# Kernel tuning notes

Measured on AMD Instinct MI355X. Metric: run time of the kernel, lower is better.

## Reference

```python
import jax, jax.numpy as jnp
import numpy as np

B, S, D, L = 32, 4096, 1024, 1

def setup_inputs() -> dict:
    key = jax.random.key(0)
    ks = jax.random.split(key, 9)
    sc = 1.0 / np.sqrt(D)
    return {
        "encoder_outputs": jax.random.normal(ks[0], (B, S, D), jnp.float32),
        "decoder_hidden_state": jax.random.normal(ks[1], (L, B, D), jnp.float32),
        "attn_mask": jax.random.randint(ks[2], (B, S), 0, 2) > 0,
        "Wa_w": jax.random.normal(ks[3], (D, D), jnp.float32) * sc,
        "Wa_b": jax.random.normal(ks[4], (D,), jnp.float32) * sc,
        "Ua_w": jax.random.normal(ks[5], (D, D), jnp.float32) * sc,
        "Ua_b": jax.random.normal(ks[6], (D,), jnp.float32) * sc,
        "Va_w": jax.random.normal(ks[7], (1, D), jnp.float32) * sc,
        "Va_b": jax.random.normal(ks[8], (1,), jnp.float32) * sc,
    }

def reference(encoder_outputs, decoder_hidden_state, attn_mask,
              Wa_w, Wa_b, Ua_w, Ua_b, Va_w, Va_b):
    # Ua(decoder_hidden_state): [L,B,D] -> transpose(0,1) -> [B,L,D] -> keep layer 0 -> [B,1,D]
    dec = jnp.einsum('lbd,ed->lbe', decoder_hidden_state, Ua_w) + Ua_b
    dec = jnp.transpose(dec, (1, 0, 2))[:, 0:1, :]            # [B,1,D]
    # Wa(encoder_outputs): [B,S,D]
    enc = jnp.einsum('bsd,ed->bse', encoder_outputs, Wa_w) + Wa_b
    # scores = Va(tanh(enc + dec)) -> [B,S,1] -> [B,1,S]
    scores = jnp.einsum('bsd,od->bso', jnp.tanh(enc + dec), Va_w) + Va_b
    scores = scores[:, :, 0][:, None, :]                      # [B,1,S]
    scores = jnp.where(attn_mask[:, None, :], scores, -jnp.inf)
    weights = jax.nn.softmax(scores, axis=-1)
    return weights
```

## Files before the change

### kernel.cpp

```cpp
#include <hip/hip_runtime.h>
#include <math.h>

#define D_DIM 1024
#define S_DIM 4096
#define B_DIM 32
#define M_TOTAL (B_DIM * S_DIM)

#define KQ   128
#define NPH  8

using short8 = __attribute__((ext_vector_type(8))) short;
using f32x4  = __attribute__((ext_vector_type(4))) float;

static __device__ __forceinline__ unsigned short f2bf(float x) {
    unsigned int u = __float_as_uint(x);
    u += 0x7fffu + ((u >> 16) & 1u);
    return (unsigned short)(u >> 16);
}

static __device__ __forceinline__ float fast_tanh(float x) {
    float e2 = __expf(2.0f * x);
    return 1.0f - 2.0f * __builtin_amdgcn_rcpf(e2 + 1.0f);
}

__global__ __launch_bounds__(256) void mask_detect_kernel(
        const unsigned int* __restrict__ m, int* __restrict__ flag) {
    __shared__ unsigned int red[4];
    int t = threadIdx.x;
    unsigned int acc = 0;
    for (int i = t; i < 32768; i += 256) acc |= (m[i] & 0xFFFFFF00u);
    #pragma unroll
    for (int k = 1; k <= 32; k <<= 1) acc |= __shfl_xor(acc, k, 64);
    if ((t & 63) == 0) red[t >> 6] = acc;
    __syncthreads();
    if (t == 0) flag[0] = ((red[0] | red[1] | red[2] | red[3]) != 0) ? 1 : 0;
}

__global__ __launch_bounds__(256) void wconv_kernel(
        const float* __restrict__ W, unsigned short* __restrict__ Wt) {
    int tid  = blockIdx.x * 256 + threadIdx.x;
    int lane = tid & 63;
    int kc   = (tid >> 6) & 31;
    int et   = tid >> 11;
    int e = et * 16 + (lane & 15);
    int k = kc * 32 + (lane >> 4) * 8;
    const float* src = W + (size_t)e * D_DIM + k;
    float4 v0 = *(const float4*)(src);
    float4 v1 = *(const float4*)(src + 4);
    short8 pk;
    pk[0] = (short)f2bf(v0.x); pk[1] = (short)f2bf(v0.y);
    pk[2] = (short)f2bf(v0.z); pk[3] = (short)f2bf(v0.w);
    pk[4] = (short)f2bf(v1.x); pk[5] = (short)f2bf(v1.y);
    pk[6] = (short)f2bf(v1.z); pk[7] = (short)f2bf(v1.w);
    *(short8*)(Wt + (size_t)tid * 8) = pk;
}

__global__ __launch_bounds__(256) void off_kernel(
        const float* __restrict__ h, const float* __restrict__ Uw,
        const float* __restrict__ Ub, const float* __restrict__ Wab,
        float* __restrict__ off) {
    int wg   = blockIdx.x * 4 + (threadIdx.x >> 6);
    int lane = threadIdx.x & 63;
    int b = wg >> 10, e = wg & 1023;
    const float4* h4 = (const float4*)(h + (size_t)b * D_DIM);
    const float4* u4 = (const float4*)(Uw + (size_t)e * D_DIM);
    float s = 0.f;
    #pragma unroll
    for (int c = 0; c < 4; ++c) {
        float4 a = h4[c * 64 + lane];
        float4 w = u4[c * 64 + lane];
        s += a.x * w.x + a.y * w.y + a.z * w.z + a.w * w.w;
    }
    #pragma unroll
    for (int m = 32; m; m >>= 1) s += __shfl_xor(s, m, 64);
    if (lane == 0) off[b * D_DIM + e] = s + Ub[e] + Wab[e];
}

__global__ __launch_bounds__(1024, 4) void score_kernel(
        const float* __restrict__ A,
        const unsigned short* __restrict__ Wt,
        const float* __restrict__ off,
        const float* __restrict__ Va,
        float* __restrict__ scores)
{
    __shared__ short As[2][64 * KQ];
    __shared__ float score_lds[64];

    const int t    = threadIdx.x;
    const int row0 = blockIdx.x * 64;
    const int b    = row0 >> 12;

    if (t < 64) score_lds[t] = 0.f;

    const int wave = t >> 6, lane = t & 63;
    const int l15 = lane & 15, lhi = lane >> 4;
    const int e0 = wave * 64;

    const unsigned short* WtB = Wt + ((size_t)wave * 4 * 32) * 512 + (size_t)lane * 8;

    const int sr = t >> 4;
    const int sk = (t & 15) * 8;
    const float* Asrc = A + (size_t)(row0 + sr) * D_DIM + sk;
    const int sidx = sr * KQ + (sk ^ ((sr & 7) << 3));

    f32x4 acc[4][4];
    #pragma unroll
    for (int rf = 0; rf < 4; ++rf)
        #pragma unroll
        for (int cf = 0; cf < 4; ++cf) acc[rf][cf] = (f32x4){0.f, 0.f, 0.f, 0.f};

    {
        float4 v0 = *(const float4*)(Asrc + 0);
        float4 v1 = *(const float4*)(Asrc + 4);
        short8 pk;
        pk[0] = (short)f2bf(v0.x); pk[1] = (short)f2bf(v0.y);
        pk[2] = (short)f2bf(v0.z); pk[3] = (short)f2bf(v0.w);
        pk[4] = (short)f2bf(v1.x); pk[5] = (short)f2bf(v1.y);
        pk[6] = (short)f2bf(v1.z); pk[7] = (short)f2bf(v1.w);
        *(short8*)(&As[0][sidx]) = pk;
    }
    __syncthreads();

    for (int q = 0; q < NPH; ++q) {
        const int cur = q & 1;

        float4 p0, p1;
        if (q < NPH - 1) {
            p0 = *(const float4*)(Asrc + (q + 1) * KQ);
            p1 = *(const float4*)(Asrc + (q + 1) * KQ + 4);
        }

        #pragma unroll
        for (int kk = 0; kk < KQ / 32; ++kk) {
            const int k0 = kk * 32 + lhi * 8;
            const int kglob = q * 4 + kk;
            short8 af[4];
            #pragma unroll
            for (int rf = 0; rf < 4; ++rf) {
                int row = rf * 16 + l15;
                af[rf] = *(const short8*)(&As[cur][row * KQ + (k0 ^ ((row & 7) << 3))]);
            }
            short8 bfr[4];
            #pragma unroll
            for (int cf = 0; cf < 4; ++cf)
                bfr[cf] = *(const short8*)(WtB + (size_t)(cf * 32 + kglob) * 512);
            __builtin_amdgcn_s_setprio(1);
            #pragma unroll
            for (int rf = 0; rf < 4; ++rf)
                #pragma unroll
                for (int cf = 0; cf < 4; ++cf)
                    acc[rf][cf] = __builtin_amdgcn_mfma_f32_16x16x32_bf16(
                        af[rf], bfr[cf], acc[rf][cf], 0, 0, 0);
            __builtin_amdgcn_s_setprio(0);
        }

        if (q < NPH - 1) {
            short8 pk;
            pk[0] = (short)f2bf(p0.x); pk[1] = (short)f2bf(p0.y);
            pk[2] = (short)f2bf(p0.z); pk[3] = (short)f2bf(p0.w);
            pk[4] = (short)f2bf(p1.x); pk[5] = (short)f2bf(p1.y);
            pk[6] = (short)f2bf(p1.z); pk[7] = (short)f2bf(p1.w);
            *(short8*)(&As[cur ^ 1][sidx]) = pk;
        }
        __syncthreads();
    }

    float sp[4][4];
    #pragma unroll
    for (int rf = 0; rf < 4; ++rf)
        #pragma unroll
        for (int j = 0; j < 4; ++j) sp[rf][j] = 0.f;

    #pragma unroll
    for (int cf = 0; cf < 4; ++cf) {
        int e = e0 + cf * 16 + l15;
        float offv = off[b * D_DIM + e];
        float vav  = Va[e];
        #pragma unroll
        for (int rf = 0; rf < 4; ++rf)
            #pragma unroll
            for (int j = 0; j < 4; ++j) {
                float x = acc[rf][cf][j] + offv;
                sp[rf][j] += fast_tanh(x) * vav;
            }
    }

    #pragma unroll
    for (int rf = 0; rf < 4; ++rf)
        #pragma unroll
        for (int j = 0; j < 4; ++j) {
            float v = sp[rf][j];
            v += __shfl_xor(v, 1, 64);
            v += __shfl_xor(v, 2, 64);
            v += __shfl_xor(v, 4, 64);
            v += __shfl_xor(v, 8, 64);
            if (l15 == 0) atomicAdd(&score_lds[rf * 16 + lhi * 4 + j], v);
        }
    __syncthreads();

    if (t < 64) scores[row0 + t] = score_lds[t];
}

__global__ __launch_bounds__(256) void softmax_kernel(
        const float* __restrict__ scores, const void* __restrict__ mask,
        const int* __restrict__ flag, float* __restrict__ out) {
    __shared__ float red[4];
    const int b = blockIdx.x, t = threadIdx.x;
    const float* s = scores + (size_t)b * S_DIM;
    const int mode8 = flag[0];

    float v[16];
    float mx = -INFINITY;
    if (mode8) {
        const unsigned char* m = (const unsigned char*)mask + (size_t)b * S_DIM;
        #pragma unroll
        for (int i = 0; i < 16; ++i) {
            int idx = i * 256 + t;
            v[i] = m[idx] ? s[idx] : -INFINITY;
            mx = fmaxf(mx, v[i]);
        }
    } else {
        const int* m = (const int*)mask + (size_t)b * S_DIM;
        #pragma unroll
        for (int i = 0; i < 16; ++i) {
            int idx = i * 256 + t;
            v[i] = m[idx] ? s[idx] : -INFINITY;
            mx = fmaxf(mx, v[i]);
        }
    }
    #pragma unroll
    for (int k = 1; k <= 32; k <<= 1) mx = fmaxf(mx, __shfl_xor(mx, k, 64));
    if ((t & 63) == 0) red[t >> 6] = mx;
    __syncthreads();
    mx = fmaxf(fmaxf(red[0], red[1]), fmaxf(red[2], red[3]));
    __syncthreads();

    float sum = 0.f;
    #pragma unroll
    for (int i = 0; i < 16; ++i) {
        v[i] = __expf(v[i] - mx);
        sum += v[i];
    }
    #pragma unroll
    for (int k = 1; k <= 32; k <<= 1) sum += __shfl_xor(sum, k, 64);
    if ((t & 63) == 0) red[t >> 6] = sum;
    __syncthreads();
    sum = red[0] + red[1] + red[2] + red[3];
    float inv = 1.f / sum;
    #pragma unroll
    for (int i = 0; i < 16; ++i) out[(size_t)b * S_DIM + i * 256 + t] = v[i] * inv;
}

extern "C" void kernel_launch(void* const* d_in, const int* in_sizes, int n_in,
                              void* d_out, int out_size, void* d_ws, size_t ws_size,
                              hipStream_t stream) {
    const float* enc  = (const float*)d_in[0];
    const float* dech = (const float*)d_in[1];
    const void*  mask = d_in[2];
    const float* Wa_w = (const float*)d_in[3];
    const float* Wa_b = (const float*)d_in[4];
    const float* Ua_w = (const float*)d_in[5];
    const float* Ua_b = (const float*)d_in[6];
    const float* Va_w = (const float*)d_in[7];
    float* out = (float*)d_out;

    char* ws = (char*)d_ws;
    unsigned short* Wt = (unsigned short*)ws;
    float* off    = (float*)(ws + (1u << 21));
    float* scores = (float*)(ws + (1u << 21) + (1u << 17));
    int*   flag   = (int*)(ws + (1u << 21) + (1u << 17) + (1u << 19));

    hipLaunchKernelGGL(mask_detect_kernel, dim3(1), dim3(256), 0, stream,
                       (const unsigned int*)mask, flag);
    hipLaunchKernelGGL(wconv_kernel, dim3(512), dim3(256), 0, stream, Wa_w, Wt);
    hipLaunchKernelGGL(off_kernel, dim3(8192), dim3(256), 0, stream,
                       dech, Ua_w, Ua_b, Wa_b, off);
    hipLaunchKernelGGL(score_kernel, dim3(2048), dim3(1024), 0, stream,
                       enc, Wt, off, Va_w, scores);
    hipLaunchKernelGGL(softmax_kernel, dim3(B_DIM), dim3(256), 0, stream,
                       scores, mask, flag, out);
}
```

Before: 376.7 us.

## Split score GEMM N dimension across two 512-thread blocks with XCD-aware block mapping

The score kernel now uses 512-thread blocks, each covering half of the 1024 output columns. Every block writes partial scores to its own buffer, and the softmax kernel adds the two halves. Block IDs are remapped so neighbouring row tiles land on the same XCD (bid&7). The B-fragment loads are also interleaved with the MFMAs to cut register pressure. Each A tile is now loaded and converted to bf16 twice, once per half, which doubles global reads of the encoder outputs in exchange for smaller blocks and more of them.

New measurement: 379.7 us. Within noise of the previous version (+0.8%).

```diff
diff --git a/kernel.cpp b/kernel.cpp
--- a/kernel.cpp
+++ b/kernel.cpp
@@ -76,7 +76,7 @@
     if (lane == 0) off[b * D_DIM + e] = s + Ub[e] + Wab[e];
 }
 
-__global__ __launch_bounds__(1024, 4) void score_kernel(
+__global__ __launch_bounds__(512, 4) void score_kernel(
         const float* __restrict__ A,
         const unsigned short* __restrict__ Wt,
         const float* __restrict__ off,
@@ -86,22 +86,28 @@
     __shared__ short As[2][64 * KQ];
     __shared__ float score_lds[64];
 
-    const int t    = threadIdx.x;
-    const int row0 = blockIdx.x * 64;
+    const int bid  = blockIdx.x;
+    const int pr   = (bid & 7) * 256 + ((bid >> 3) >> 1);
+    const int h    = (bid >> 3) & 1;
+    const int row0 = pr * 64;
     const int b    = row0 >> 12;
 
+    const int t = threadIdx.x;
     if (t < 64) score_lds[t] = 0.f;
 
     const int wave = t >> 6, lane = t & 63;
     const int l15 = lane & 15, lhi = lane >> 4;
-    const int e0 = wave * 64;
-
-    const unsigned short* WtB = Wt + ((size_t)wave * 4 * 32) * 512 + (size_t)lane * 8;
-
-    const int sr = t >> 4;
-    const int sk = (t & 15) * 8;
+    const int e0 = h * 512 + wave * 64;
+
+    const unsigned short* WtB =
+        Wt + ((size_t)(h * 32 + wave * 4) * 32) * 512 + (size_t)lane * 8;
+
+    const int sr = t >> 3;
+    const int sk = (t & 7) * 16;
     const float* Asrc = A + (size_t)(row0 + sr) * D_DIM + sk;
-    const int sidx = sr * KQ + (sk ^ ((sr & 7) << 3));
+    const int swz   = (sr & 7) << 3;
+    const int sidx0 = sr * KQ + (sk ^ swz);
+    const int sidx1 = sr * KQ + ((sk + 8) ^ swz);
 
     f32x4 acc[4][4];
     #pragma unroll
@@ -112,22 +118,32 @@
     {
         float4 v0 = *(const float4*)(Asrc + 0);
         float4 v1 = *(const float4*)(Asrc + 4);
-        short8 pk;
-        pk[0] = (short)f2bf(v0.x); pk[1] = (short)f2bf(v0.y);
-        pk[2] = (short)f2bf(v0.z); pk[3] = (short)f2bf(v0.w);
-        pk[4] = (short)f2bf(v1.x); pk[5] = (short)f2bf(v1.y);
-        pk[6] = (short)f2bf(v1.z); pk[7] = (short)f2bf(v1.w);
-        *(short8*)(&As[0][sidx]) = pk;
+        float4 v2 = *(const float4*)(Asrc + 8);
+        float4 v3 = *(const float4*)(Asrc + 12);
+        short8 pk0, pk1;
+        pk0[0] = (short)f2bf(v0.x); pk0[1] = (short)f2bf(v0.y);
+        pk0[2] = (short)f2bf(v0.z); pk0[3] = (short)f2bf(v0.w);
+        pk0[4] = (short)f2bf(v1.x); pk0[5] = (short)f2bf(v1.y);
+        pk0[6] = (short)f2bf(v1.z); pk0[7] = (short)f2bf(v1.w);
+        pk1[0] = (short)f2bf(v2.x); pk1[1] = (short)f2bf(v2.y);
+        pk1[2] = (short)f2bf(v2.z); pk1[3] = (short)f2bf(v2.w);
+        pk1[4] = (short)f2bf(v3.x); pk1[5] = (short)f2bf(v3.y);
+        pk1[6] = (short)f2bf(v3.z); pk1[7] = (short)f2bf(v3.w);
+        *(short8*)(&As[0][sidx0]) = pk0;
+        *(short8*)(&As[0][sidx1]) = pk1;
     }
     __syncthreads();
 
     for (int q = 0; q < NPH; ++q) {
         const int cur = q & 1;
 
-        float4 p0, p1;
+        float4 p0, p1, p2, p3;
         if (q < NPH - 1) {
-            p0 = *(const float4*)(Asrc + (q + 1) * KQ);
-            p1 = *(const float4*)(Asrc + (q + 1) * KQ + 4);
+            const float* nx = Asrc + (q + 1) * KQ;
+            p0 = *(const float4*)(nx + 0);
+            p1 = *(const float4*)(nx + 4);
+            p2 = *(const float4*)(nx + 8);
+            p3 = *(const float4*)(nx + 12);
         }
 
         #pragma unroll
@@ -140,27 +156,30 @@
                 int row = rf * 16 + l15;
                 af[rf] = *(const short8*)(&As[cur][row * KQ + (k0 ^ ((row & 7) << 3))]);
             }
-            short8 bfr[4];
-            #pragma unroll
-            for (int cf = 0; cf < 4; ++cf)
-                bfr[cf] = *(const short8*)(WtB + (size_t)(cf * 32 + kglob) * 512);
             __builtin_amdgcn_s_setprio(1);
             #pragma unroll
-            for (int rf = 0; rf < 4; ++rf)
+            for (int cf = 0; cf < 4; ++cf) {
+                short8 bfr = *(const short8*)(WtB + (size_t)(cf * 32 + kglob) * 512);
                 #pragma unroll
-                for (int cf = 0; cf < 4; ++cf)
+                for (int rf = 0; rf < 4; ++rf)
                     acc[rf][cf] = __builtin_amdgcn_mfma_f32_16x16x32_bf16(
-                        af[rf], bfr[cf], acc[rf][cf], 0, 0, 0);
+                        af[rf], bfr, acc[rf][cf], 0, 0, 0);
+            }
             __builtin_amdgcn_s_setprio(0);
         }
 
         if (q < NPH - 1) {
-            short8 pk;
-            pk[0] = (short)f2bf(p0.x); pk[1] = (short)f2bf(p0.y);
-            pk[2] = (short)f2bf(p0.z); pk[3] = (short)f2bf(p0.w);
-            pk[4] = (short)f2bf(p1.x); pk[5] = (short)f2bf(p1.y);
-            pk[6] = (short)f2bf(p1.z); pk[7] = (short)f2bf(p1.w);
-            *(short8*)(&As[cur ^ 1][sidx]) = pk;
+            short8 pk0, pk1;
+            pk0[0] = (short)f2bf(p0.x); pk0[1] = (short)f2bf(p0.y);
+            pk0[2] = (short)f2bf(p0.z); pk0[3] = (short)f2bf(p0.w);
+            pk0[4] = (short)f2bf(p1.x); pk0[5] = (short)f2bf(p1.y);
+            pk0[6] = (short)f2bf(p1.z); pk0[7] = (short)f2bf(p1.w);
+            pk1[0] = (short)f2bf(p2.x); pk1[1] = (short)f2bf(p2.y);
+            pk1[2] = (short)f2bf(p2.z); pk1[3] = (short)f2bf(p2.w);
+            pk1[4] = (short)f2bf(p3.x); pk1[5] = (short)f2bf(p3.y);
+            pk1[6] = (short)f2bf(p3.z); pk1[7] = (short)f2bf(p3.w);
+            *(short8*)(&As[cur ^ 1][sidx0]) = pk0;
+            *(short8*)(&As[cur ^ 1][sidx1]) = pk1;
         }
         __syncthreads();
     }
@@ -198,7 +217,7 @@
         }
     __syncthreads();
 
-    if (t < 64) scores[row0 + t] = score_lds[t];
+    if (t < 64) scores[(size_t)h * M_TOTAL + row0 + t] = score_lds[t];
 }
 
 __global__ __launch_bounds__(256) void softmax_kernel(
@@ -206,7 +225,8 @@
         const int* __restrict__ flag, float* __restrict__ out) {
     __shared__ float red[4];
     const int b = blockIdx.x, t = threadIdx.x;
-    const float* s = scores + (size_t)b * S_DIM;
+    const float* s0 = scores + (size_t)b * S_DIM;
+    const float* s1 = scores + (size_t)M_TOTAL + (size_t)b * S_DIM;
     const int mode8 = flag[0];
 
     float v[16];
@@ -216,7 +236,7 @@
         #pragma unroll
         for (int i = 0; i < 16; ++i) {
             int idx = i * 256 + t;
-            v[i] = m[idx] ? s[idx] : -INFINITY;
+            v[i] = m[idx] ? (s0[idx] + s1[idx]) : -INFINITY;
             mx = fmaxf(mx, v[i]);
         }
     } else {
@@ -224,7 +244,7 @@
         #pragma unroll
         for (int i = 0; i < 16; ++i) {
             int idx = i * 256 + t;
-            v[i] = m[idx] ? s[idx] : -INFINITY;
+            v[i] = m[idx] ? (s0[idx] + s1[idx]) : -INFINITY;
             mx = fmaxf(mx, v[i]);
         }
     }
@@ -268,14 +288,14 @@
     unsigned short* Wt = (unsigned short*)ws;
     float* off    = (float*)(ws + (1u << 21));
     float* scores = (float*)(ws + (1u << 21) + (1u << 17));
-    int*   flag   = (int*)(ws + (1u << 21) + (1u << 17) + (1u << 19));
+    int*   flag   = (int*)(ws + (1u << 21) + (1u << 17) + (1u << 20));
 
     hipLaunchKernelGGL(mask_detect_kernel, dim3(1), dim3(256), 0, stream,
                        (const unsigned int*)mask, flag);
     hipLaunchKernelGGL(wconv_kernel, dim3(512), dim3(256), 0, stream, Wa_w, Wt);
     hipLaunchKernelGGL(off_kernel, dim3(8192), dim3(256), 0, stream,
                        dech, Ua_w, Ua_b, Wa_b, off);
-    hipLaunchKernelGGL(score_kernel, dim3(2048), dim3(1024), 0, stream,
+    hipLaunchKernelGGL(score_kernel, dim3(4096), dim3(512), 0, stream,
                        enc, Wt, off, Va_w, scores);
     hipLaunchKernelGGL(softmax_kernel, dim3(B_DIM), dim3(256), 0, stream,
                        scores, mask, flag, out);
```

## Split score GEMM N-dimension across four 256-thread blocks with atomic score reduction

Applied to the files above, without the earlier changes.

The 1024-thread block that covered all 1024 output columns is split into four 256-thread blocks, each covering a quarter of the columns. Their partial Va-dot scores are accumulated with global atomics into a buffer that a new zero kernel clears first. Block IDs are remapped so blocks sharing the same A rows run close together, B fragments are double-buffered one k-step ahead, and fp32-to-bf16 packing uses the paired conversion intrinsic. The aim is higher occupancy and more latency hiding. The cost is that each A tile is now loaded and converted four times, plus extra atomic traffic and one more launch.

Result: slower. 503.9 us (+33.8%).

```diff
diff --git a/kernel.cpp b/kernel.cpp
--- a/kernel.cpp
+++ b/kernel.cpp
@@ -1,4 +1,5 @@
 #include <hip/hip_runtime.h>
+#include <hip/hip_bf16.h>
 #include <math.h>
 
 #define D_DIM 1024
@@ -16,6 +17,11 @@
     unsigned int u = __float_as_uint(x);
     u += 0x7fffu + ((u >> 16) & 1u);
     return (unsigned short)(u >> 16);
+}
+
+static __device__ __forceinline__ unsigned int pk2(float lo, float hi) {
+    __hip_bfloat162 h = __float22bfloat162_rn(float2{lo, hi});
+    unsigned int u; __builtin_memcpy(&u, &h, 4); return u;
 }
 
 static __device__ __forceinline__ float fast_tanh(float x) {
@@ -76,7 +82,11 @@
     if (lane == 0) off[b * D_DIM + e] = s + Ub[e] + Wab[e];
 }
 
-__global__ __launch_bounds__(1024, 4) void score_kernel(
+__global__ __launch_bounds__(256) void zero_kernel(float* __restrict__ p) {
+    ((float4*)p)[blockIdx.x * 256 + threadIdx.x] = (float4){0.f, 0.f, 0.f, 0.f};
+}
+
+__global__ __launch_bounds__(256, 3) void score_kernel(
         const float* __restrict__ A,
         const unsigned short* __restrict__ Wt,
         const float* __restrict__ off,
@@ -86,22 +96,30 @@
     __shared__ short As[2][64 * KQ];
     __shared__ float score_lds[64];
 
-    const int t    = threadIdx.x;
-    const int row0 = blockIdx.x * 64;
+    const int bid  = blockIdx.x;
+    const int pr   = (bid & 7) * 256 + (bid >> 5);
+    const int qr   = (bid >> 3) & 3;
+    const int row0 = pr * 64;
     const int b    = row0 >> 12;
 
+    const int t = threadIdx.x;
     if (t < 64) score_lds[t] = 0.f;
 
     const int wave = t >> 6, lane = t & 63;
     const int l15 = lane & 15, lhi = lane >> 4;
-    const int e0 = wave * 64;
-
-    const unsigned short* WtB = Wt + ((size_t)wave * 4 * 32) * 512 + (size_t)lane * 8;
-
-    const int sr = t >> 4;
-    const int sk = (t & 15) * 8;
+    const int e0 = qr * 256 + wave * 64;
+
+    const unsigned short* WtB =
+        Wt + ((size_t)(qr * 16 + wave * 4) * 32) * 512 + (size_t)lane * 8;
+
+    const int sr = t >> 2;
+    const int sk = (t & 3) * 32;
     const float* Asrc = A + (size_t)(row0 + sr) * D_DIM + sk;
-    const int sidx = sr * KQ + (sk ^ ((sr & 7) << 3));
+    const int swz = (sr & 7) << 3;
+    const int sidx0 = sr * KQ + ((sk +  0) ^ swz);
+    const int sidx1 = sr * KQ + ((sk +  8) ^ swz);
+    const int sidx2 = sr * KQ + ((sk + 16) ^ swz);
+    const int sidx3 = sr * KQ + ((sk + 24) ^ swz);
 
     f32x4 acc[4][4];
     #pragma unroll
@@ -109,58 +127,97 @@
         #pragma unroll
         for (int cf = 0; cf < 4; ++cf) acc[rf][cf] = (f32x4){0.f, 0.f, 0.f, 0.f};
 
+    short8 B0[4], B1[4];
+
+    #define MF(KK, USE, PRE, STAGE_CODE) do {                                 \
+        const int kgn_ = (q * 4 + KK + 1 < 32) ? q * 4 + KK + 1 : 31;         \
+        _Pragma("unroll")                                                     \
+        for (int cf = 0; cf < 4; ++cf)                                        \
+            PRE[cf] = *(const short8*)(WtB + (size_t)(cf * 32 + kgn_) * 512); \
+        STAGE_CODE                                                            \
+        short8 af[4];                                                         \
+        const int k0_ = KK * 32 + lhi * 8;                                    \
+        _Pragma("unroll")                                                     \
+        for (int rf = 0; rf < 4; ++rf) {                                      \
+            int row = rf * 16 + l15;                                          \
+            af[rf] = *(const short8*)(&As[cur][row * KQ                       \
+                       + (k0_ ^ ((row & 7) << 3))]);                          \
+        }                                                                     \
+        __builtin_amdgcn_s_setprio(1);                                        \
+        _Pragma("unroll")                                                     \
+        for (int rf = 0; rf < 4; ++rf)                                        \
+            _Pragma("unroll")                                                 \
+            for (int cf = 0; cf < 4; ++cf)                                    \
+                acc[rf][cf] = __builtin_amdgcn_mfma_f32_16x16x32_bf16(        \
+                    af[rf], USE[cf], acc[rf][cf], 0, 0, 0);                   \
+        __builtin_amdgcn_s_setprio(0);                                        \
+    } while (0)
+
     {
-        float4 v0 = *(const float4*)(Asrc + 0);
-        float4 v1 = *(const float4*)(Asrc + 4);
-        short8 pk;
-        pk[0] = (short)f2bf(v0.x); pk[1] = (short)f2bf(v0.y);
-        pk[2] = (short)f2bf(v0.z); pk[3] = (short)f2bf(v0.w);
-        pk[4] = (short)f2bf(v1.x); pk[5] = (short)f2bf(v1.y);
-        pk[6] = (short)f2bf(v1.z); pk[7] = (short)f2bf(v1.w);
-        *(short8*)(&As[0][sidx]) = pk;
-    }
+        float4 v0 = *(const float4*)(Asrc +  0);
+        float4 v1 = *(const float4*)(Asrc +  4);
+        float4 v2 = *(const float4*)(Asrc +  8);
+        float4 v3 = *(const float4*)(Asrc + 12);
+        float4 v4 = *(const float4*)(Asrc + 16);
+        float4 v5 = *(const float4*)(Asrc + 20);
+        float4 v6 = *(const float4*)(Asrc + 24);
+        float4 v7 = *(const float4*)(Asrc + 28);
+        uint4 o;
+        o.x = pk2(v0.x, v0.y); o.y = pk2(v0.z, v0.w);
+        o.z = pk2(v1.x, v1.y); o.w = pk2(v1.z, v1.w);
+        *(uint4*)(&As[0][sidx0]) = o;
+        o.x = pk2(v2.x, v2.y); o.y = pk2(v2.z, v2.w);
+        o.z = pk2(v3.x, v3.y); o.w = pk2(v3.z, v3.w);
+        *(uint4*)(&As[0][sidx1]) = o;
+        o.x = pk2(v4.x, v4.y); o.y = pk2(v4.z, v4.w);
+        o.z = pk2(v5.x, v5.y); o.w = pk2(v5.z, v5.w);
+        *(uint4*)(&As[0][sidx2]) = o;
+        o.x = pk2(v6.x, v6.y); o.y = pk2(v6.z, v6.w);
+        o.z = pk2(v7.x, v7.y); o.w = pk2(v7.z, v7.w);
+        *(uint4*)(&As[0][sidx3]) = o;
+    }
+    #pragma unroll
+    for (int cf = 0; cf < 4; ++cf)
+        B0[cf] = *(const short8*)(WtB + (size_t)(cf * 32 + 0) * 512);
     __syncthreads();
 
     for (int q = 0; q < NPH; ++q) {
         const int cur = q & 1;
-
-        float4 p0, p1;
+        float4 p0, p1, p2, p3, p4, p5, p6, p7;
+
+        MF(0, B0, B1, );
+        MF(1, B1, B0,
+           if (q < NPH - 1) {
+               const float* nx = Asrc + (q + 1) * KQ;
+               p0 = *(const float4*)(nx +  0);
+               p1 = *(const float4*)(nx +  4);
+               p2 = *(const float4*)(nx +  8);
+               p3 = *(const float4*)(nx + 12);
+           });
+        MF(2, B0, B1,
+           if (q < NPH - 1) {
+               const float* nx = Asrc + (q + 1) * KQ;
+               p4 = *(const float4*)(nx + 16);
+               p5 = *(const float4*)(nx + 20);
+               p6 = *(const float4*)(nx + 24);
+               p7 = *(const float4*)(nx + 28);
+           });
+        MF(3, B1, B0, );
+
         if (q < NPH - 1) {
-            p0 = *(const float4*)(Asrc + (q + 1) * KQ);
-            p1 = *(const float4*)(Asrc + (q + 1) * KQ + 4);
-        }
-
-        #pragma unroll
-        for (int kk = 0; kk < KQ / 32; ++kk) {
-            const int k0 = kk * 32 + lhi * 8;
-            const int kglob = q * 4 + kk;
-            short8 af[4];
-            #pragma unroll
-            for (int rf = 0; rf < 4; ++rf) {
-                int row = rf * 16 + l15;
-                af[rf] = *(const short8*)(&As[cur][row * KQ + (k0 ^ ((row & 7) << 3))]);
-            }
-            short8 bfr[4];
-            #pragma unroll
-            for (int cf = 0; cf < 4; ++cf)
-                bfr[cf] = *(const short8*)(WtB + (size_t)(cf * 32 + kglob) * 512);
-            __builtin_amdgcn_s_setprio(1);
-            #pragma unroll
-            for (int rf = 0; rf < 4; ++rf)
-                #pragma unroll
-                for (int cf = 0; cf < 4; ++cf)
-                    acc[rf][cf] = __builtin_amdgcn_mfma_f32_16x16x32_bf16(
-                        af[rf], bfr[cf], acc[rf][cf], 0, 0, 0);
-            __builtin_amdgcn_s_setprio(0);
-        }
-
-        if (q < NPH - 1) {
-            short8 pk;
-            pk[0] = (short)f2bf(p0.x); pk[1] = (short)f2bf(p0.y);
-            pk[2] = (short)f2bf(p0.z); pk[3] = (short)f2bf(p0.w);
-            pk[4] = (short)f2bf(p1.x); pk[5] = (short)f2bf(p1.y);
-            pk[6] = (short)f2bf(p1.z); pk[7] = (short)f2bf(p1.w);
-            *(short8*)(&As[cur ^ 1][sidx]) = pk;
+            uint4 o;
+            o.x = pk2(p0.x, p0.y); o.y = pk2(p0.z, p0.w);
+            o.z = pk2(p1.x, p1.y); o.w = pk2(p1.z, p1.w);
+            *(uint4*)(&As[cur ^ 1][sidx0]) = o;
+            o.x = pk2(p2.x, p2.y); o.y = pk2(p2.z, p2.w);
+            o.z = pk2(p3.x, p3.y); o.w = pk2(p3.z, p3.w);
+            *(uint4*)(&As[cur ^ 1][sidx1]) = o;
+            o.x = pk2(p4.x, p4.y); o.y = pk2(p4.z, p4.w);
+            o.z = pk2(p5.x, p5.y); o.w = pk2(p5.z, p5.w);
+            *(uint4*)(&As[cur ^ 1][sidx2]) = o;
+            o.x = pk2(p6.x, p6.y); o.y = pk2(p6.z, p6.w);
+            o.z = pk2(p7.x, p7.y); o.w = pk2(p7.z, p7.w);
+            *(uint4*)(&As[cur ^ 1][sidx3]) = o;
         }
         __syncthreads();
     }
@@ -198,7 +255,7 @@
         }
     __syncthreads();
 
-    if (t < 64) scores[row0 + t] = score_lds[t];
+    if (t < 64) atomicAdd(&scores[row0 + t], score_lds[t]);
 }
 
 __global__ __launch_bounds__(256) void softmax_kernel(
@@ -275,7 +332,8 @@
     hipLaunchKernelGGL(wconv_kernel, dim3(512), dim3(256), 0, stream, Wa_w, Wt);
     hipLaunchKernelGGL(off_kernel, dim3(8192), dim3(256), 0, stream,
                        dech, Ua_w, Ua_b, Wa_b, off);
-    hipLaunchKernelGGL(score_kernel, dim3(2048), dim3(1024), 0, stream,
+    hipLaunchKernelGGL(zero_kernel, dim3(128), dim3(256), 0, stream, scores);
+    hipLaunchKernelGGL(score_kernel, dim3(8192), dim3(256), 0, stream,
                        enc, Wt, off, Va_w, scores);
     hipLaunchKernelGGL(softmax_kernel, dim3(B_DIM), dim3(256), 0, stream,
                        scores, mask, flag, out);
```

## Retile score GEMM into 256x256 blocks split over the output dimension

Applied to the files above, without the earlier changes.

The score kernel moves from 64-row tiles spanning all 1024 output columns to 256-row by 256-column tiles with 512 threads. Each wave now computes 128x64, so A fragments are reused across more MFMAs. The four column quarters are combined with global atomicAdd into a scores buffer that a new zero kernel clears first. The K loop uses 64-wide double-buffered stages, prefetches B fragments in registers, converts with packed bf16 intrinsics, and orders blocks so the four column tiles of one row panel run close together. The cost is that the fp32 encoder tile is read from global memory four times (hopefully from L2) and an extra launch plus atomics are added.

Result: slower. 563.7 us (+49.7%).

```diff
diff --git a/kernel.cpp b/kernel.cpp
--- a/kernel.cpp
+++ b/kernel.cpp
@@ -1,4 +1,5 @@
 #include <hip/hip_runtime.h>
+#include <hip/hip_bf16.h>
 #include <math.h>
 
 #define D_DIM 1024
@@ -6,9 +7,6 @@
 #define B_DIM 32
 #define M_TOTAL (B_DIM * S_DIM)
 
-#define KQ   128
-#define NPH  8
-
 using short8 = __attribute__((ext_vector_type(8))) short;
 using f32x4  = __attribute__((ext_vector_type(4))) float;
 
@@ -16,6 +14,11 @@
     unsigned int u = __float_as_uint(x);
     u += 0x7fffu + ((u >> 16) & 1u);
     return (unsigned short)(u >> 16);
+}
+
+static __device__ __forceinline__ unsigned int pk2(float lo, float hi) {
+    __hip_bfloat162 h = __float22bfloat162_rn(float2{lo, hi});
+    unsigned int u; __builtin_memcpy(&u, &h, 4); return u;
 }
 
 static __device__ __forceinline__ float fast_tanh(float x) {
@@ -76,108 +79,158 @@
     if (lane == 0) off[b * D_DIM + e] = s + Ub[e] + Wab[e];
 }
 
-__global__ __launch_bounds__(1024, 4) void score_kernel(
+__global__ __launch_bounds__(256) void zero_kernel(float* __restrict__ p) {
+    ((float4*)p)[blockIdx.x * 256 + threadIdx.x] = (float4){0.f, 0.f, 0.f, 0.f};
+}
+
+__global__ __launch_bounds__(512, 2) void score_kernel(
         const float* __restrict__ A,
         const unsigned short* __restrict__ Wt,
         const float* __restrict__ off,
         const float* __restrict__ Va,
         float* __restrict__ scores)
 {
-    __shared__ short As[2][64 * KQ];
-    __shared__ float score_lds[64];
-
-    const int t    = threadIdx.x;
-    const int row0 = blockIdx.x * 64;
-    const int b    = row0 >> 12;
-
-    if (t < 64) score_lds[t] = 0.f;
+    __shared__ short As[2][256 * 64];
+    __shared__ float score_lds[256];
+
+    const int bid   = blockIdx.x;
+    const int idx   = bid >> 3;
+    const int panel = (bid & 7) * 64 + (idx >> 2);
+    const int colq  = idx & 3;
+    const int row0  = panel * 256;
+    const int b     = panel >> 4;
+
+    const int t = threadIdx.x;
+    if (t < 256) score_lds[t] = 0.f;
 
     const int wave = t >> 6, lane = t & 63;
     const int l15 = lane & 15, lhi = lane >> 4;
-    const int e0 = wave * 64;
-
-    const unsigned short* WtB = Wt + ((size_t)wave * 4 * 32) * 512 + (size_t)lane * 8;
-
-    const int sr = t >> 4;
-    const int sk = (t & 15) * 8;
-    const float* Asrc = A + (size_t)(row0 + sr) * D_DIM + sk;
-    const int sidx = sr * KQ + (sk ^ ((sr & 7) << 3));
-
-    f32x4 acc[4][4];
-    #pragma unroll
-    for (int rf = 0; rf < 4; ++rf)
+    const int wr = wave >> 2;
+    const int wc = wave & 3;
+    const int et0 = colq * 16 + wc * 4;
+
+    const int sr = t >> 1;
+    const int kh = (t & 1) * 32;
+    const float* asrc = A + (size_t)(row0 + sr) * D_DIM + kh;
+    const int swz = (sr & 7) << 4;
+
+    f32x4 acc[8][4];
+    #pragma unroll
+    for (int rf = 0; rf < 8; ++rf)
         #pragma unroll
         for (int cf = 0; cf < 4; ++cf) acc[rf][cf] = (f32x4){0.f, 0.f, 0.f, 0.f};
 
+    short8 bA[4], bB[4];
+
+    #define LOADB(SET, KC) do {                                              \
+        _Pragma("unroll")                                                    \
+        for (int cf = 0; cf < 4; ++cf)                                       \
+            SET[cf] = *(const short8*)(Wt                                    \
+                + ((size_t)((et0 + cf) * 32 + (KC))) * 512 + lane * 8);      \
+    } while (0)
+
+    #define KGSTEP(KG, BFR) do {                                             \
+        short8 af[8];                                                        \
+        _Pragma("unroll")                                                    \
+        for (int rf = 0; rf < 8; ++rf) {                                     \
+            int row = wr * 128 + rf * 16 + l15;                              \
+            af[rf] = *(const short8*)((const char*)As[cur] + row * 128       \
+                       + (((KG) * 64 + lhi * 16) ^ ((row & 7) << 4)));       \
+        }                                                                    \
+        __builtin_amdgcn_s_setprio(1);                                       \
+        _Pragma("unroll")                                                    \
+        for (int rf = 0; rf < 8; ++rf)                                       \
+            _Pragma("unroll")                                                \
+            for (int cf = 0; cf < 4; ++cf)                                   \
+                acc[rf][cf] = __builtin_amdgcn_mfma_f32_16x16x32_bf16(       \
+                    af[rf], BFR[cf], acc[rf][cf], 0, 0, 0);                  \
+        __builtin_amdgcn_s_setprio(0);                                       \
+    } while (0)
+
+    #define CVT2(P0, P1, BYTECOL) do {                                       \
+        uint4 o_;                                                            \
+        o_.x = pk2(P0.x, P0.y); o_.y = pk2(P0.z, P0.w);                      \
+        o_.z = pk2(P1.x, P1.y); o_.w = pk2(P1.z, P1.w);                      \
+        *(uint4*)((char*)As[cur ^ 1] + sr * 128 + ((BYTECOL) ^ swz)) = o_;   \
+    } while (0)
+
     {
-        float4 v0 = *(const float4*)(Asrc + 0);
-        float4 v1 = *(const float4*)(Asrc + 4);
-        short8 pk;
-        pk[0] = (short)f2bf(v0.x); pk[1] = (short)f2bf(v0.y);
-        pk[2] = (short)f2bf(v0.z); pk[3] = (short)f2bf(v0.w);
-        pk[4] = (short)f2bf(v1.x); pk[5] = (short)f2bf(v1.y);
-        pk[6] = (short)f2bf(v1.z); pk[7] = (short)f2bf(v1.w);
-        *(short8*)(&As[0][sidx]) = pk;
-    }
-    __syncthreads();
-
-    for (int q = 0; q < NPH; ++q) {
-        const int cur = q & 1;
-
-        float4 p0, p1;
-        if (q < NPH - 1) {
-            p0 = *(const float4*)(Asrc + (q + 1) * KQ);
-            p1 = *(const float4*)(Asrc + (q + 1) * KQ + 4);
-        }
-
-        #pragma unroll
-        for (int kk = 0; kk < KQ / 32; ++kk) {
-            const int k0 = kk * 32 + lhi * 8;
-            const int kglob = q * 4 + kk;
-            short8 af[4];
-            #pragma unroll
-            for (int rf = 0; rf < 4; ++rf) {
-                int row = rf * 16 + l15;
-                af[rf] = *(const short8*)(&As[cur][row * KQ + (k0 ^ ((row & 7) << 3))]);
-            }
-            short8 bfr[4];
-            #pragma unroll
-            for (int cf = 0; cf < 4; ++cf)
-                bfr[cf] = *(const short8*)(WtB + (size_t)(cf * 32 + kglob) * 512);
-            __builtin_amdgcn_s_setprio(1);
-            #pragma unroll
-            for (int rf = 0; rf < 4; ++rf)
-                #pragma unroll
-                for (int cf = 0; cf < 4; ++cf)
-                    acc[rf][cf] = __builtin_amdgcn_mfma_f32_16x16x32_bf16(
-                        af[rf], bfr[cf], acc[rf][cf], 0, 0, 0);
-            __builtin_amdgcn_s_setprio(0);
-        }
-
-        if (q < NPH - 1) {
-            short8 pk;
-            pk[0] = (short)f2bf(p0.x); pk[1] = (short)f2bf(p0.y);
-            pk[2] = (short)f2bf(p0.z); pk[3] = (short)f2bf(p0.w);
-            pk[4] = (short)f2bf(p1.x); pk[5] = (short)f2bf(p1.y);
-            pk[6] = (short)f2bf(p1.z); pk[7] = (short)f2bf(p1.w);
-            *(short8*)(&As[cur ^ 1][sidx]) = pk;
+        float4 v0 = *(const float4*)(asrc + 0);
+        float4 v1 = *(const float4*)(asrc + 4);
+        float4 v2 = *(const float4*)(asrc + 8);
+        float4 v3 = *(const float4*)(asrc + 12);
+        float4 v4 = *(const float4*)(asrc + 16);
+        float4 v5 = *(const float4*)(asrc + 20);
+        float4 v6 = *(const float4*)(asrc + 24);
+        float4 v7 = *(const float4*)(asrc + 28);
+        uint4 o;
+        char* dst = (char*)As[0] + sr * 128;
+        o.x = pk2(v0.x, v0.y); o.y = pk2(v0.z, v0.w);
+        o.z = pk2(v1.x, v1.y); o.w = pk2(v1.z, v1.w);
+        *(uint4*)(dst + ((kh * 2 +  0) ^ swz)) = o;
+        o.x = pk2(v2.x, v2.y); o.y = pk2(v2.z, v2.w);
+        o.z = pk2(v3.x, v3.y); o.w = pk2(v3.z, v3.w);
+        *(uint4*)(dst + ((kh * 2 + 16) ^ swz)) = o;
+        o.x = pk2(v4.x, v4.y); o.y = pk2(v4.z, v4.w);
+        o.z = pk2(v5.x, v5.y); o.w = pk2(v5.z, v5.w);
+        *(uint4*)(dst + ((kh * 2 + 32) ^ swz)) = o;
+        o.x = pk2(v6.x, v6.y); o.y = pk2(v6.z, v6.w);
+        o.z = pk2(v7.x, v7.y); o.w = pk2(v7.z, v7.w);
+        *(uint4*)(dst + ((kh * 2 + 48) ^ swz)) = o;
+    }
+    LOADB(bA, 0);
+    __syncthreads();
+
+    for (int tile = 0; tile < 16; ++tile) {
+        const int cur = tile & 1;
+        const float* nx = asrc + (tile + 1) * 64;
+
+        float4 q0, q1, q2, q3;
+        if (tile < 15) {
+            q0 = *(const float4*)(nx + 0);
+            q1 = *(const float4*)(nx + 4);
+            q2 = *(const float4*)(nx + 8);
+            q3 = *(const float4*)(nx + 12);
+        }
+        LOADB(bB, tile * 2 + 1);
+
+        KGSTEP(0, bA);
+
+        if (tile < 15) {
+            CVT2(q0, q1, kh * 2 + 0);
+            CVT2(q2, q3, kh * 2 + 16);
+        }
+        float4 q4, q5, q6, q7;
+        if (tile < 15) {
+            q4 = *(const float4*)(nx + 16);
+            q5 = *(const float4*)(nx + 20);
+            q6 = *(const float4*)(nx + 24);
+            q7 = *(const float4*)(nx + 28);
+            LOADB(bA, (tile + 1) * 2);
+        }
+
+        KGSTEP(1, bB);
+
+        if (tile < 15) {
+            CVT2(q4, q5, kh * 2 + 32);
+            CVT2(q6, q7, kh * 2 + 48);
         }
         __syncthreads();
     }
 
-    float sp[4][4];
-    #pragma unroll
-    for (int rf = 0; rf < 4; ++rf)
+    float sp[8][4];
+    #pragma unroll
+    for (int rf = 0; rf < 8; ++rf)
         #pragma unroll
         for (int j = 0; j < 4; ++j) sp[rf][j] = 0.f;
 
     #pragma unroll
     for (int cf = 0; cf < 4; ++cf) {
-        int e = e0 + cf * 16 + l15;
+        int e = colq * 256 + wc * 64 + cf * 16 + l15;
         float offv = off[b * D_DIM + e];
         float vav  = Va[e];
         #pragma unroll
-        for (int rf = 0; rf < 4; ++rf)
+        for (int rf = 0; rf < 8; ++rf)
             #pragma unroll
             for (int j = 0; j < 4; ++j) {
                 float x = acc[rf][cf][j] + offv;
@@ -186,7 +239,7 @@
     }
 
     #pragma unroll
-    for (int rf = 0; rf < 4; ++rf)
+    for (int rf = 0; rf < 8; ++rf)
         #pragma unroll
         for (int j = 0; j < 4; ++j) {
             float v = sp[rf][j];
@@ -194,11 +247,12 @@
             v += __shfl_xor(v, 2, 64);
             v += __shfl_xor(v, 4, 64);
             v += __shfl_xor(v, 8, 64);
-            if (l15 == 0) atomicAdd(&score_lds[rf * 16 + lhi * 4 + j], v);
-        }
-    __syncthreads();
-
-    if (t < 64) scores[row0 + t] = score_lds[t];
+            if (l15 == 0)
+                atomicAdd(&score_lds[wr * 128 + rf * 16 + lhi * 4 + j], v);
+        }
+    __syncthreads();
+
+    if (t < 256) atomicAdd(&scores[row0 + t], score_lds[t]);
 }
 
 __global__ __launch_bounds__(256) void softmax_kernel(
@@ -275,7 +329,8 @@
     hipLaunchKernelGGL(wconv_kernel, dim3(512), dim3(256), 0, stream, Wa_w, Wt);
     hipLaunchKernelGGL(off_kernel, dim3(8192), dim3(256), 0, stream,
                        dech, Ua_w, Ua_b, Wa_b, off);
-    hipLaunchKernelGGL(score_kernel, dim3(2048), dim3(1024), 0, stream,
+    hipLaunchKernelGGL(zero_kernel, dim3(128), dim3(256), 0, stream, scores);
+    hipLaunchKernelGGL(score_kernel, dim3(2048), dim3(512), 0, stream,
                        enc, Wt, off, Va_w, scores);
     hipLaunchKernelGGL(softmax_kernel, dim3(B_DIM), dim3(256), 0, stream,
                        scores, mask, flag, out);
```
